# Optimization experiments

Measured on AMD Instinct MI355X. Metric: run time of the kernel, lower is better.

Reference implementation:

```python
import jax, jax.numpy as jnp
import numpy as np

N_HEAD = 16
N_EMBD = 64  # per-head dim in this module's convention
INNER = N_HEAD * N_EMBD  # 1024


def setup_inputs() -> dict:
    key = jax.random.key(0)
    ks = jax.random.split(key, 6)
    B, S = 4, 2048
    scale = 0.02
    return {
        "x": jax.random.normal(ks[0], (B, S, N_EMBD), dtype=jnp.float32),
        "Wq": jax.random.normal(ks[1], (N_EMBD, INNER), dtype=jnp.float32) * scale,
        "Wk": jax.random.normal(ks[2], (N_EMBD, INNER), dtype=jnp.float32) * scale,
        "Wv": jax.random.normal(ks[3], (N_EMBD, INNER), dtype=jnp.float32) * scale,
        "Wo": jax.random.normal(ks[4], (INNER, N_EMBD), dtype=jnp.float32) * scale,
        "bo": jax.random.normal(ks[5], (N_EMBD,), dtype=jnp.float32) * scale,
        "causal_mask": 1,
    }


def reference(x, Wq, Wk, Wv, Wo, bo, causal_mask):
    B, S, _ = x.shape
    # projections: [B,S,INNER] -> [B,H,S,D]
    def split_heads(t):
        return t.reshape(B, S, N_HEAD, N_EMBD).transpose(0, 2, 1, 3)
    q = split_heads(x @ Wq)
    k = split_heads(x @ Wk)
    v = split_heads(x @ Wv)
    # [B,H,S,S]
    scores = jnp.einsum("bhqd,bhkd->bhqk", q, k) / jnp.sqrt(jnp.float32(N_EMBD))
    if causal_mask:
        future = jnp.triu(jnp.ones((S, S), dtype=scores.dtype), k=1)
        scores = scores - 1e9 * future  # matches torch: subtract 1e9*mask
    attn = jax.nn.softmax(scores, axis=-1)
    out = jnp.einsum("bhqk,bhkd->bhqd", attn, v)
    out = out.transpose(0, 2, 1, 3).reshape(B, S, INNER)
    return out @ Wo + bo
```

## Files before the change

### kernel.cpp

```cpp
#include <hip/hip_runtime.h>
#include <hip/hip_bf16.h>

#define NHEAD 16
#define HDIM 64
#define DINNER 1024
#define NBATCH 4
#define SEQ 2048
#define NTOK (NBATCH*SEQ)

typedef __bf16 bf16;
typedef __bf16 bf16x4 __attribute__((ext_vector_type(4)));
typedef __bf16 bf16x8 __attribute__((ext_vector_type(8)));
typedef float f32x4 __attribute__((ext_vector_type(4)));

#define OFF_BO   8
#define OFF_XB   128
#define OFF_WQT  (OFF_XB + NTOK*HDIM)
#define OFF_WKT  (OFF_WQT + DINNER*HDIM)
#define OFF_WVT  (OFF_WKT + DINNER*HDIM)
#define OFF_WOT  (OFF_WVT + DINNER*HDIM)
#define OFF_Q    (OFF_WOT + DINNER*HDIM)
#define OFF_K    (OFF_Q + NTOK*DINNER)
#define OFF_VT   (OFF_K + NTOK*DINNER)
#define OFF_ATT  (OFF_VT + NTOK*DINNER)
#define OFF_ATT2 (OFF_ATT + NTOK*DINNER)
#define OFF_L    (OFF_ATT2 + NTOK*DINNER)

#define SSCALE 0.18033688011112042f

static __device__ __forceinline__ bf16x8 ld8(const bf16* p) {
  return *reinterpret_cast<const bf16x8*>(p);
}

static __device__ __forceinline__ int detect_isbf(const void* x, int tid,
                                                  int* sflag) {
  if (tid < 64) {
    const unsigned short* xb = (const unsigned short*)x;
    bool ok = true;
#pragma unroll
    for (int i = 0; i < 8; i++) {
      unsigned e = (xb[tid * 8 + i] >> 7) & 0xFF;
      ok = ok && (e >= 64 && e <= 140);
    }
    unsigned long long mball = __ballot(ok);
    if (tid == 0) *sflag = (mball == ~0ull) ? 1 : 0;
  }
  __syncthreads();
  return *sflag;
}

__global__ __launch_bounds__(256) void prep_kernel(
    const void* __restrict__ x, const void* __restrict__ Wq,
    const void* __restrict__ Wk, const void* __restrict__ Wv,
    const void* __restrict__ Wo, const void* __restrict__ bo,
    bf16* __restrict__ ws) {
  __shared__ int sflag;
  int isbf = detect_isbf(x, threadIdx.x, &sflag);
  int z = blockIdx.y;
  int idx = blockIdx.x * 256 + threadIdx.x;
  if (z < 3) {
    const void* src = (z == 0) ? Wq : (z == 1) ? Wk : Wv;
    bf16* dst = ws + ((z == 0) ? OFF_WQT : (z == 1) ? OFF_WKT : OFF_WVT);
    int d = idx >> 10, n = idx & 1023;
    float v = isbf ? (float)((const bf16*)src)[idx] : ((const float*)src)[idx];
    if (z == 0) v *= SSCALE;
    dst[n * HDIM + d] = (bf16)v;
  } else if (z == 3) {
    int k = idx >> 6, n = idx & 63;
    float v = isbf ? (float)((const bf16*)Wo)[idx] : ((const float*)Wo)[idx];
    ws[OFF_WOT + n * DINNER + k] = (bf16)v;
  } else if (z == 4) {
    int i = idx * 8;
    bf16x8 v;
    if (isbf) {
      v = ld8((const bf16*)x + i);
    } else {
      f32x4 a = *reinterpret_cast<const f32x4*>((const float*)x + i);
      f32x4 b2 = *reinterpret_cast<const f32x4*>((const float*)x + i + 4);
#pragma unroll
      for (int j = 0; j < 4; j++) { v[j] = (bf16)a[j]; v[4 + j] = (bf16)b2[j]; }
    }
    *reinterpret_cast<bf16x8*>(&ws[OFF_XB + i]) = v;
  } else {
    if (idx < 64) ws[OFF_BO + idx] = isbf ? ((const bf16*)bo)[idx] : (bf16)((const float*)bo)[idx];
  }
}

__global__ __launch_bounds__(256) void qkv_kernel(bf16* __restrict__ ws) {
  __shared__ __align__(16) bf16 Vst[4][16 * 72];
  int tt = blockIdx.x, pz = blockIdx.z;
  int w = threadIdx.x >> 6;
  int nc = blockIdx.y * 4 + w;
  int lane = threadIdx.x & 63;
  int lq = lane & 15, quad = lane >> 4;
  const bf16* WT = ws + OFF_WQT + pz * (DINNER * HDIM);
  int n0 = nc * 64;
  bf16x8 w0[4], w1[4];
#pragma unroll
  for (int c = 0; c < 4; c++) {
    const bf16* wr = WT + (n0 + c * 16 + lq) * HDIM;
    w0[c] = ld8(wr + quad * 8);
    w1[c] = ld8(wr + 32 + quad * 8);
  }
  bf16* Qb = ws + OFF_Q;
  bf16* Kb = ws + OFF_K;
  bf16* VTb = ws + OFF_VT;
  bf16x8 ao0[4], ao1[4];
  if (pz == 2) {
    const bf16* WoT = ws + OFF_WOT;
#pragma unroll
    for (int c = 0; c < 4; c++) {
      const bf16* orow = WoT + (size_t)(c * 16 + lq) * DINNER + nc * 64;
      ao0[c] = ld8(orow + quad * 8);
      ao1[c] = ld8(orow + 32 + quad * 8);
    }
  }
#pragma unroll
  for (int mi = 0; mi < 4; mi++) {
    int t0 = tt * 64 + mi * 16;
    const bf16* xrow = ws + OFF_XB + (t0 + lq) * HDIM;
    bf16x8 x0 = ld8(xrow + quad * 8);
    bf16x8 x1 = ld8(xrow + 32 + quad * 8);
    int b = t0 >> 11, s0 = t0 & (SEQ - 1);
    if (pz < 2) {
#pragma unroll
      for (int c = 0; c < 4; c++) {
        f32x4 z = {0.f, 0.f, 0.f, 0.f};
        z = __builtin_amdgcn_mfma_f32_16x16x32_bf16(w0[c], x0, z, 0, 0, 0);
        z = __builtin_amdgcn_mfma_f32_16x16x32_bf16(w1[c], x1, z, 0, 0, 0);
        bf16x4 pk = {(bf16)z[0], (bf16)z[1], (bf16)z[2], (bf16)z[3]};
        bf16* P = (pz == 0) ? Qb : Kb;
        *reinterpret_cast<bf16x4*>(
            &P[((size_t)(b * NHEAD + nc) * SEQ + s0 + lq) * HDIM + c * 16 + quad * 4]) = pk;
      }
    } else {
#pragma unroll
      for (int c = 0; c < 4; c++) {
        f32x4 z = {0.f, 0.f, 0.f, 0.f};
        z = __builtin_amdgcn_mfma_f32_16x16x32_bf16(w0[c], x0, z, 0, 0, 0);
        z = __builtin_amdgcn_mfma_f32_16x16x32_bf16(w1[c], x1, z, 0, 0, 0);
        bf16x4 pk = {(bf16)z[0], (bf16)z[1], (bf16)z[2], (bf16)z[3]};
        *reinterpret_cast<bf16x4*>(&Vst[w][lq * 72 + c * 16 + quad * 4]) = pk;
      }
      bf16x8 bv0 = ld8(&Vst[w][lq * 72 + quad * 8]);
      bf16x8 bv1 = ld8(&Vst[w][lq * 72 + 32 + quad * 8]);
#pragma unroll
      for (int c = 0; c < 4; c++) {
        f32x4 z2 = {0.f, 0.f, 0.f, 0.f};
        z2 = __builtin_amdgcn_mfma_f32_16x16x32_bf16(ao0[c], bv0, z2, 0, 0, 0);
        z2 = __builtin_amdgcn_mfma_f32_16x16x32_bf16(ao1[c], bv1, z2, 0, 0, 0);
#pragma unroll
        for (int r = 0; r < 4; r++) {
          int d = c * 16 + quad * 4 + r;
          VTb[(((size_t)b * NHEAD + nc) * HDIM + d) * SEQ + s0 + lq] = (bf16)z2[r];
        }
      }
    }
  }
}

__global__ __launch_bounds__(256, 2) void flash_kernel(const int* __restrict__ cmask,
                                                       bf16* __restrict__ ws) {
  __shared__ __align__(16) bf16 Kl[2][64 * 64];
  __shared__ __align__(16) bf16 Vl[2][64 * 64];
  __shared__ __align__(16) bf16 Pl[4][16 * 64];
  int bid = blockIdx.x;
  int bh = (bid & 7) * 8 + ((bid >> 3) & 7);
  int z = (bid >> 6) & 7;
  int half = bid >> 9;
  int w = threadIdx.x >> 6;
  int lane = threadIdx.x & 63;
  int lq = lane & 15, quad = lane >> 4;
  int causal = cmask[0];
  const bf16* Q = ws + OFF_Q + (size_t)bh * SEQ * HDIM;
  const bf16* K = ws + OFF_K + (size_t)bh * SEQ * HDIM;
  const bf16* VT = ws + OFF_VT + (size_t)bh * HDIM * SEQ;
  int b = bh >> 4, h = bh & 15;
  bf16* ar = ws + OFF_ATT + (size_t)half * NTOK * DINNER;
  float* Lp = reinterpret_cast<float*>(ws + OFF_L) + (size_t)half * NTOK * NHEAD;
  int sr = threadIdx.x >> 2;
  int sg = (threadIdx.x & 3) * 16;
  int sc0 = (((threadIdx.x & 3) * 2) ^ (sr & 7)) << 3;
  int sc1 = (((threadIdx.x & 3) * 2 + 1) ^ (sr & 7)) << 3;
  int rq0 = (quad ^ (lq & 7)) << 3;
  int rq1 = ((4 + quad) ^ (lq & 7)) << 3;

  int bufc = 0;

  for (int seg = 0; seg < 2; ++seg) {
    int qt = seg ? (15 - z) : z;
    int Ts = causal ? (seg ? (32 - 2 * z) : (2 * z + 2)) : 32;
    int hs = Ts >> 1;
    int t0 = half * hs, t1 = t0 + hs;
    int qb = qt * 128;
    int qw = qb + w * 32;

    bf16x8 bq[2][2];
#pragma unroll
    for (int m = 0; m < 2; m++) {
      const bf16* qrow = Q + (qw + m * 16 + lq) * HDIM;
      bq[m][0] = ld8(qrow + quad * 8);
      bq[m][1] = ld8(qrow + 32 + quad * 8);
    }
    f32x4 o[2][4];
    float lsum[2] = {0.f, 0.f};
#pragma unroll
    for (int m = 0; m < 2; m++)
#pragma unroll
      for (int c = 0; c < 4; c++) o[m][c] = (f32x4){0.f, 0.f, 0.f, 0.f};

    bf16x8 kst0 = ld8(K + (size_t)(t0 * 64 + sr) * HDIM + sg);
    bf16x8 kst1 = ld8(K + (size_t)(t0 * 64 + sr) * HDIM + sg + 8);
    bf16x8 vst0 = ld8(VT + (size_t)sr * SEQ + t0 * 64 + sg);
    bf16x8 vst1 = ld8(VT + (size_t)sr * SEQ + t0 * 64 + sg + 8);

    for (int ti = t0; ti < t1; ++ti, ++bufc) {
      int buf = bufc & 1;
      int k0 = ti * 64;
      *reinterpret_cast<bf16x8*>(&Kl[buf][sr * 64 + sc0]) = kst0;
      *reinterpret_cast<bf16x8*>(&Kl[buf][sr * 64 + sc1]) = kst1;
      *reinterpret_cast<bf16x8*>(&Vl[buf][sr * 64 + sc0]) = vst0;
      *reinterpret_cast<bf16x8*>(&Vl[buf][sr * 64 + sc1]) = vst1;
      int kn = (ti + 1 < t1) ? (k0 + 64) : k0;
      kst0 = ld8(K + (size_t)(kn + sr) * HDIM + sg);
      kst1 = ld8(K + (size_t)(kn + sr) * HDIM + sg + 8);
      vst0 = ld8(VT + (size_t)sr * SEQ + kn + sg);
      vst1 = ld8(VT + (size_t)sr * SEQ + kn + sg + 8);
      __syncthreads();
      if (causal && k0 > qw + 31) continue;
      f32x4 st[2][4];
#pragma unroll
      for (int t = 0; t < 4; t++) {
        bf16x8 a0 = ld8(&Kl[buf][(t * 16 + lq) * 64 + rq0]);
        bf16x8 a1 = ld8(&Kl[buf][(t * 16 + lq) * 64 + rq1]);
#pragma unroll
        for (int m = 0; m < 2; m++) {
          f32x4 zz = {0.f, 0.f, 0.f, 0.f};
          zz = __builtin_amdgcn_mfma_f32_16x16x32_bf16(a0, bq[m][0], zz, 0, 0, 0);
          zz = __builtin_amdgcn_mfma_f32_16x16x32_bf16(a1, bq[m][1], zz, 0, 0, 0);
          st[m][t] = zz;
        }
      }
      bool needmask = causal && (k0 + 63 > qw);
      bf16x8 bp[2][2];
#pragma unroll
      for (int m = 0; m < 2; m++) {
        if (needmask) {
          int qrel = qw + m * 16 + lq - k0 - quad * 4;
#pragma unroll
          for (int t = 0; t < 4; t++)
#pragma unroll
            for (int r = 0; r < 4; r++)
              if (t * 16 + r > qrel) st[m][t][r] = -200.0f;
        }
        float sum = 0.f;
#pragma unroll
        for (int t = 0; t < 4; t++) {
          float e0 = exp2f(st[m][t][0]);
          float e1 = exp2f(st[m][t][1]);
          float e2 = exp2f(st[m][t][2]);
          float e3 = exp2f(st[m][t][3]);
          sum += (e0 + e1) + (e2 + e3);
          bf16x4 pk = {(bf16)e0, (bf16)e1, (bf16)e2, (bf16)e3};
          int ch = ((t * 2 + (quad >> 1)) ^ (lq & 7)) << 3;
          *reinterpret_cast<bf16x4*>(&Pl[w][lq * 64 + ch + (quad & 1) * 4]) = pk;
        }
        lsum[m] += sum;
        bp[m][0] = ld8(&Pl[w][lq * 64 + rq0]);
        bp[m][1] = ld8(&Pl[w][lq * 64 + rq1]);
      }
#pragma unroll
      for (int c = 0; c < 4; c++) {
        bf16x8 av0 = ld8(&Vl[buf][(c * 16 + lq) * 64 + rq0]);
        bf16x8 av1 = ld8(&Vl[buf][(c * 16 + lq) * 64 + rq1]);
#pragma unroll
        for (int m = 0; m < 2; m++) {
          o[m][c] = __builtin_amdgcn_mfma_f32_16x16x32_bf16(av0, bp[m][0], o[m][c], 0, 0, 0);
          o[m][c] = __builtin_amdgcn_mfma_f32_16x16x32_bf16(av1, bp[m][1], o[m][c], 0, 0, 0);
        }
      }
    }
#pragma unroll
    for (int m = 0; m < 2; m++) {
      lsum[m] += __shfl_xor(lsum[m], 16);
      lsum[m] += __shfl_xor(lsum[m], 32);
      size_t row = (size_t)(b * SEQ + qw + m * 16 + lq);
      if (quad == 0) Lp[row * NHEAD + h] = lsum[m];
      size_t rowoff = row * DINNER + (size_t)h * HDIM;
#pragma unroll
      for (int c = 0; c < 4; c++) {
        bf16x4 ov = {(bf16)o[m][c][0], (bf16)o[m][c][1],
                     (bf16)o[m][c][2], (bf16)o[m][c][3]};
        *reinterpret_cast<bf16x4*>(&ar[rowoff + c * 16 + quad * 4]) = ov;
      }
    }
  }
}

__global__ __launch_bounds__(256) void reduce_kernel(const bf16* __restrict__ ws,
                                                     const void* __restrict__ x,
                                                     void* __restrict__ outp) {
  __shared__ int sflag;
  int isbf = detect_isbf(x, threadIdx.x, &sflag);
  int idx = blockIdx.x * 256 + threadIdx.x;
  int t = idx >> 6, d = idx & 63;
  const bf16* a0 = ws + OFF_ATT + (size_t)t * DINNER + d;
  const bf16* a1 = a0 + (size_t)NTOK * DINNER;
  const float* l0 = reinterpret_cast<const float*>(ws + OFF_L) + (size_t)t * NHEAD;
  const float* l1 = l0 + (size_t)NTOK * NHEAD;
  float s = (float)ws[OFF_BO + d];
#pragma unroll
  for (int h = 0; h < 16; h++) {
    float inv = 1.0f / (l0[h] + l1[h]);
    s += ((float)a0[h * 64] + (float)a1[h * 64]) * inv;
  }
  if (isbf) ((bf16*)outp)[idx] = (bf16)s;
  else      ((float*)outp)[idx] = s;
}

extern "C" void kernel_launch(void* const* d_in, const int* in_sizes, int n_in,
                              void* d_out, int out_size, void* d_ws, size_t ws_size,
                              hipStream_t stream) {
  const void* x  = d_in[0];
  const void* Wq = d_in[1];
  const void* Wk = d_in[2];
  const void* Wv = d_in[3];
  const void* Wo = d_in[4];
  const void* bo = d_in[5];
  const int* cm  = (const int*)d_in[6];
  bf16* ws = (bf16*)d_ws;

  hipLaunchKernelGGL(prep_kernel, dim3(256, 6), dim3(256), 0, stream,
                     x, Wq, Wk, Wv, Wo, bo, ws);
  hipLaunchKernelGGL(qkv_kernel, dim3(128, 4, 3), dim3(256), 0, stream, ws);
  hipLaunchKernelGGL(flash_kernel, dim3(1024), dim3(256), 0, stream, cm, ws);
  hipLaunchKernelGGL(reduce_kernel, dim3(2048), dim3(256), 0, stream, ws, x, d_out);
}
```

Baseline: 164.1 us.

## Switch flash kernel to 32x32x16 MFMA with register-only P via permlane32 swap

The flash attention inner loop now uses 32x32x16 bf16 MFMAs instead of 16x16x32, with each wave covering 32 query rows in a single f32x16 accumulator pair. The softmax probabilities are repacked in registers with permlane32_swap to form the B operand of the PV MFMA, which removes the per-wave LDS P buffer and its store/load round trip. It also wraps the MFMA blocks in s_setprio to favour matrix issue. The masking index math and output/L store layout are rewritten for the new accumulator layout, so any mistake in that mapping would give wrong results. The larger accumulators may also raise register pressure.

```diff
diff --git a/kernel.cpp b/kernel.cpp
--- a/kernel.cpp
+++ b/kernel.cpp
@@ -9,9 +9,14 @@
 #define NTOK (NBATCH*SEQ)
 
 typedef __bf16 bf16;
+typedef __bf16 bf16x2 __attribute__((ext_vector_type(2)));
 typedef __bf16 bf16x4 __attribute__((ext_vector_type(4)));
 typedef __bf16 bf16x8 __attribute__((ext_vector_type(8)));
 typedef float f32x4 __attribute__((ext_vector_type(4)));
+typedef float f32x16 __attribute__((ext_vector_type(16)));
+typedef unsigned int u32;
+typedef unsigned int u32x2 __attribute__((ext_vector_type(2)));
+typedef unsigned int u32x4 __attribute__((ext_vector_type(4)));
 
 #define OFF_BO   8
 #define OFF_XB   128
@@ -30,6 +35,11 @@
 
 static __device__ __forceinline__ bf16x8 ld8(const bf16* p) {
   return *reinterpret_cast<const bf16x8*>(p);
+}
+
+static __device__ __forceinline__ u32 pkbf(float a, float b) {
+  bf16x2 t; t[0] = (bf16)a; t[1] = (bf16)b;
+  return __builtin_bit_cast(u32, t);
 }
 
 static __device__ __forceinline__ int detect_isbf(const void* x, int tid,
@@ -163,14 +173,13 @@
                                                        bf16* __restrict__ ws) {
   __shared__ __align__(16) bf16 Kl[2][64 * 64];
   __shared__ __align__(16) bf16 Vl[2][64 * 64];
-  __shared__ __align__(16) bf16 Pl[4][16 * 64];
   int bid = blockIdx.x;
   int bh = (bid & 7) * 8 + ((bid >> 3) & 7);
   int z = (bid >> 6) & 7;
   int half = bid >> 9;
   int w = threadIdx.x >> 6;
   int lane = threadIdx.x & 63;
-  int lq = lane & 15, quad = lane >> 4;
+  int ql = lane & 31, lh = lane >> 5, l7 = lane & 7;
   int causal = cmask[0];
   const bf16* Q = ws + OFF_Q + (size_t)bh * SEQ * HDIM;
   const bf16* K = ws + OFF_K + (size_t)bh * SEQ * HDIM;
@@ -182,8 +191,6 @@
   int sg = (threadIdx.x & 3) * 16;
   int sc0 = (((threadIdx.x & 3) * 2) ^ (sr & 7)) << 3;
   int sc1 = (((threadIdx.x & 3) * 2 + 1) ^ (sr & 7)) << 3;
-  int rq0 = (quad ^ (lq & 7)) << 3;
-  int rq1 = ((4 + quad) ^ (lq & 7)) << 3;
 
   int bufc = 0;
 
@@ -194,20 +201,17 @@
     int t0 = half * hs, t1 = t0 + hs;
     int qb = qt * 128;
     int qw = qb + w * 32;
-
-    bf16x8 bq[2][2];
-#pragma unroll
-    for (int m = 0; m < 2; m++) {
-      const bf16* qrow = Q + (qw + m * 16 + lq) * HDIM;
-      bq[m][0] = ld8(qrow + quad * 8);
-      bq[m][1] = ld8(qrow + 32 + quad * 8);
-    }
-    f32x4 o[2][4];
-    float lsum[2] = {0.f, 0.f};
-#pragma unroll
-    for (int m = 0; m < 2; m++)
-#pragma unroll
-      for (int c = 0; c < 4; c++) o[m][c] = (f32x4){0.f, 0.f, 0.f, 0.f};
+    int qa = qw + ql;
+
+    bf16x8 bq[4];
+#pragma unroll
+    for (int dsub = 0; dsub < 4; dsub++)
+      bq[dsub] = ld8(Q + (size_t)qa * HDIM + dsub * 16 + lh * 8);
+
+    f32x16 o0, o1;
+#pragma unroll
+    for (int r = 0; r < 16; r++) { o0[r] = 0.f; o1[r] = 0.f; }
+    float lsum = 0.f;
 
     bf16x8 kst0 = ld8(K + (size_t)(t0 * 64 + sr) * HDIM + sg);
     bf16x8 kst1 = ld8(K + (size_t)(t0 * 64 + sr) * HDIM + sg + 8);
@@ -228,71 +232,88 @@
       vst1 = ld8(VT + (size_t)sr * SEQ + kn + sg + 8);
       __syncthreads();
       if (causal && k0 > qw + 31) continue;
-      f32x4 st[2][4];
-#pragma unroll
-      for (int t = 0; t < 4; t++) {
-        bf16x8 a0 = ld8(&Kl[buf][(t * 16 + lq) * 64 + rq0]);
-        bf16x8 a1 = ld8(&Kl[buf][(t * 16 + lq) * 64 + rq1]);
-#pragma unroll
-        for (int m = 0; m < 2; m++) {
-          f32x4 zz = {0.f, 0.f, 0.f, 0.f};
-          zz = __builtin_amdgcn_mfma_f32_16x16x32_bf16(a0, bq[m][0], zz, 0, 0, 0);
-          zz = __builtin_amdgcn_mfma_f32_16x16x32_bf16(a1, bq[m][1], zz, 0, 0, 0);
-          st[m][t] = zz;
+
+      f32x16 s0, s1;
+#pragma unroll
+      for (int r = 0; r < 16; r++) { s0[r] = 0.f; s1[r] = 0.f; }
+      __builtin_amdgcn_s_setprio(1);
+#pragma unroll
+      for (int dsub = 0; dsub < 4; dsub++) {
+        int co = ((dsub * 2 + lh) ^ l7) << 3;
+        bf16x8 a0 = ld8(&Kl[buf][ql * 64 + co]);
+        bf16x8 a1 = ld8(&Kl[buf][(32 + ql) * 64 + co]);
+        s0 = __builtin_amdgcn_mfma_f32_32x32x16_bf16(a0, bq[dsub], s0, 0, 0, 0);
+        s1 = __builtin_amdgcn_mfma_f32_32x32x16_bf16(a1, bq[dsub], s1, 0, 0, 0);
+      }
+      __builtin_amdgcn_s_setprio(0);
+
+      if (causal && (k0 + 63 > qw)) {
+#pragma unroll
+        for (int r = 0; r < 16; r++) {
+          int kk = k0 + (r & 3) + 8 * (r >> 2) + 4 * lh;
+          if (kk > qa) s0[r] = -200.0f;
+          if (kk + 32 > qa) s1[r] = -200.0f;
         }
       }
-      bool needmask = causal && (k0 + 63 > qw);
-      bf16x8 bp[2][2];
-#pragma unroll
-      for (int m = 0; m < 2; m++) {
-        if (needmask) {
-          int qrel = qw + m * 16 + lq - k0 - quad * 4;
-#pragma unroll
-          for (int t = 0; t < 4; t++)
-#pragma unroll
-            for (int r = 0; r < 4; r++)
-              if (t * 16 + r > qrel) st[m][t][r] = -200.0f;
+
+      bf16x8 pf[4];
+      {
+        float e[16];
+#pragma unroll
+        for (int r = 0; r < 16; r++) { e[r] = exp2f(s0[r]); lsum += e[r]; }
+#pragma unroll
+        for (int j = 0; j < 2; j++) {
+          u32 x0 = pkbf(e[8 * j + 0], e[8 * j + 1]);
+          u32 x1 = pkbf(e[8 * j + 2], e[8 * j + 3]);
+          u32 y0 = pkbf(e[8 * j + 4], e[8 * j + 5]);
+          u32 y1 = pkbf(e[8 * j + 6], e[8 * j + 7]);
+          u32x2 r0 = __builtin_amdgcn_permlane32_swap(x0, y0, false, false);
+          u32x2 r1 = __builtin_amdgcn_permlane32_swap(x1, y1, false, false);
+          u32x4 fw = {r0[0], r1[0], r0[1], r1[1]};
+          pf[j] = __builtin_bit_cast(bf16x8, fw);
         }
-        float sum = 0.f;
-#pragma unroll
-        for (int t = 0; t < 4; t++) {
-          float e0 = exp2f(st[m][t][0]);
-          float e1 = exp2f(st[m][t][1]);
-          float e2 = exp2f(st[m][t][2]);
-          float e3 = exp2f(st[m][t][3]);
-          sum += (e0 + e1) + (e2 + e3);
-          bf16x4 pk = {(bf16)e0, (bf16)e1, (bf16)e2, (bf16)e3};
-          int ch = ((t * 2 + (quad >> 1)) ^ (lq & 7)) << 3;
-          *reinterpret_cast<bf16x4*>(&Pl[w][lq * 64 + ch + (quad & 1) * 4]) = pk;
+      }
+      {
+        float e[16];
+#pragma unroll
+        for (int r = 0; r < 16; r++) { e[r] = exp2f(s1[r]); lsum += e[r]; }
+#pragma unroll
+        for (int j = 0; j < 2; j++) {
+          u32 x0 = pkbf(e[8 * j + 0], e[8 * j + 1]);
+          u32 x1 = pkbf(e[8 * j + 2], e[8 * j + 3]);
+          u32 y0 = pkbf(e[8 * j + 4], e[8 * j + 5]);
+          u32 y1 = pkbf(e[8 * j + 6], e[8 * j + 7]);
+          u32x2 r0 = __builtin_amdgcn_permlane32_swap(x0, y0, false, false);
+          u32x2 r1 = __builtin_amdgcn_permlane32_swap(x1, y1, false, false);
+          u32x4 fw = {r0[0], r1[0], r0[1], r1[1]};
+          pf[2 + j] = __builtin_bit_cast(bf16x8, fw);
         }
-        lsum[m] += sum;
-        bp[m][0] = ld8(&Pl[w][lq * 64 + rq0]);
-        bp[m][1] = ld8(&Pl[w][lq * 64 + rq1]);
-      }
-#pragma unroll
-      for (int c = 0; c < 4; c++) {
-        bf16x8 av0 = ld8(&Vl[buf][(c * 16 + lq) * 64 + rq0]);
-        bf16x8 av1 = ld8(&Vl[buf][(c * 16 + lq) * 64 + rq1]);
-#pragma unroll
-        for (int m = 0; m < 2; m++) {
-          o[m][c] = __builtin_amdgcn_mfma_f32_16x16x32_bf16(av0, bp[m][0], o[m][c], 0, 0, 0);
-          o[m][c] = __builtin_amdgcn_mfma_f32_16x16x32_bf16(av1, bp[m][1], o[m][c], 0, 0, 0);
-        }
-      }
-    }
-#pragma unroll
-    for (int m = 0; m < 2; m++) {
-      lsum[m] += __shfl_xor(lsum[m], 16);
-      lsum[m] += __shfl_xor(lsum[m], 32);
-      size_t row = (size_t)(b * SEQ + qw + m * 16 + lq);
-      if (quad == 0) Lp[row * NHEAD + h] = lsum[m];
-      size_t rowoff = row * DINNER + (size_t)h * HDIM;
-#pragma unroll
-      for (int c = 0; c < 4; c++) {
-        bf16x4 ov = {(bf16)o[m][c][0], (bf16)o[m][c][1],
-                     (bf16)o[m][c][2], (bf16)o[m][c][3]};
-        *reinterpret_cast<bf16x4*>(&ar[rowoff + c * 16 + quad * 4]) = ov;
-      }
+      }
+
+      __builtin_amdgcn_s_setprio(1);
+#pragma unroll
+      for (int ks = 0; ks < 4; ks++) {
+        int co = ((ks * 2 + lh) ^ l7) << 3;
+        bf16x8 av0 = ld8(&Vl[buf][ql * 64 + co]);
+        bf16x8 av1 = ld8(&Vl[buf][(32 + ql) * 64 + co]);
+        o0 = __builtin_amdgcn_mfma_f32_32x32x16_bf16(av0, pf[ks], o0, 0, 0, 0);
+        o1 = __builtin_amdgcn_mfma_f32_32x32x16_bf16(av1, pf[ks], o1, 0, 0, 0);
+      }
+      __builtin_amdgcn_s_setprio(0);
+    }
+
+    lsum += __shfl_xor(lsum, 32);
+    size_t row = (size_t)(b * SEQ) + qa;
+    if (lane < 32) Lp[row * NHEAD + h] = lsum;
+    size_t rowoff = row * DINNER + (size_t)h * HDIM;
+#pragma unroll
+    for (int g = 0; g < 4; g++) {
+      bf16x4 ov0 = {(bf16)o0[4 * g], (bf16)o0[4 * g + 1],
+                    (bf16)o0[4 * g + 2], (bf16)o0[4 * g + 3]};
+      bf16x4 ov1 = {(bf16)o1[4 * g], (bf16)o1[4 * g + 1],
+                    (bf16)o1[4 * g + 2], (bf16)o1[4 * g + 3]};
+      *reinterpret_cast<bf16x4*>(&ar[rowoff + 8 * g + 4 * lh]) = ov0;
+      *reinterpret_cast<bf16x4*>(&ar[rowoff + 32 + 8 * g + 4 * lh]) = ov1;
     }
   }
 }
```

Measured after the change: 170.3 us. +3.8%, slower.
